# Kernel optimization log

Measured on AMD Instinct MI355X. Metric: run time of the kernel, lower is better.

## Reference

```python
import jax, jax.numpy as jnp
import numpy as np

B, D, N = 131072, 512, 101
BIG = 1e9
NORM_EPS = 0.1  # F.normalize eps


def setup_inputs() -> dict:
    key = jax.random.key(0)
    k1, k2, k3 = jax.random.split(key, 3)
    embeddings = jax.random.normal(k1, (B, D), dtype=jnp.float32)
    centers_weight = jax.random.normal(k2, (N, D), dtype=jnp.float32)
    labels = jax.random.randint(k3, (B,), 0, N, dtype=jnp.int64)
    return {"embeddings": embeddings, "centers_weight": centers_weight, "labels": labels}


def reference(embeddings, centers_weight, labels):
    # ---- center (MSE) term: per-sample squared distance to own center ----
    gathered = centers_weight[labels]                     # [B, D]
    center_loss = ((embeddings - gathered) ** 2).sum(axis=1)  # [B] (reduction=None)

    # ---- margin term (original operates on .data -> detached) ----
    W = jax.lax.stop_gradient(centers_weight)
    norms = jnp.sqrt((W * W).sum(axis=1, keepdims=True))
    C = W / jnp.maximum(norms, NORM_EPS)                  # F.normalize(p=2, eps=0.1)
    n = C.shape[0]
    dist = 1.0 - C @ C.T                                  # [N, N] cosine distance
    idx = jnp.arange(n)
    diff = jnp.abs(idx[:, None] - idx[None, :])
    dist = dist + BIG * (diff == 0)                       # mask diagonal (eye)

    # neighbor distances BEFORE they are masked out
    d_lower = jnp.diagonal(dist, offset=-1)               # Dist[i, i-1], i = 1..n-1
    d_upper = jnp.diagonal(dist, offset=1)                # Dist[i, i+1], i = 0..n-2

    dist_masked = dist + BIG * (diff == 1)                # mask adjacent centers
    min_dist = dist_masked.min(axis=1)                    # Dist[i, NegIdx]

    margin = (jax.nn.relu(2.0 * d_lower - min_dist[1:]).sum()
              + jax.nn.relu(2.0 * d_upper - min_dist[:-1]).sum()) / n

    return margin + center_loss.mean()
```

## Files before the change

kernel.cpp:

```cpp
#include <hip/hip_runtime.h>

#define BB 131072
#define DD 512
#define NN 101
#define D4 128
#define TOT (BB * D4)
#define GBLK 256
#define CBLK 2048
#define STR (CBLK * 256)
#define NPAIR (NN * NN)

typedef float f4 __attribute__((ext_vector_type(4)));

__global__ __launch_bounds__(256, 8) void fused_kernel(
    const f4* __restrict__ emb, const f4* __restrict__ ctr,
    const int* __restrict__ labels,
    float* __restrict__ partial,
    float* __restrict__ G)
{
    int lane = threadIdx.x & 63;
    int wid  = threadIdx.x >> 6;

    if (blockIdx.x < GBLK) {
        int w = blockIdx.x * 4 + wid;
        for (int p = w; p < NPAIR; p += GBLK * 4) {
            int i = p / NN;
            int j = p % NN;
            const f4* wi = ctr + i * D4;
            const f4* wj = ctr + j * D4;
            float dot = 0.f;
#pragma unroll
            for (int r = 0; r < 2; r++) {
                f4 a = wi[lane + r * 64];
                f4 c = wj[lane + r * 64];
                dot += a.x * c.x + a.y * c.y + a.z * c.z + a.w * c.w;
            }
            for (int off = 32; off > 0; off >>= 1)
                dot += __shfl_down(dot, off);
            if (lane == 0) G[p] = dot;
        }
        return;
    }

    int b   = blockIdx.x - GBLK;
    int tid = b * 256 + threadIdx.x;
    int d4  = tid & (D4 - 1);
    float local = 0.f;
#pragma unroll 1
    for (int kk = 0; kk < 8; kk++) {
        int i0 = tid + (kk * 4 + 0) * STR;
        int i1 = tid + (kk * 4 + 1) * STR;
        int i2 = tid + (kk * 4 + 2) * STR;
        int i3 = tid + (kk * 4 + 3) * STR;
        int l0 = labels[i0 >> 7];
        int l1 = labels[i1 >> 7];
        int l2 = labels[i2 >> 7];
        int l3 = labels[i3 >> 7];
        f4 e0 = emb[i0];
        f4 e1 = emb[i1];
        f4 e2 = emb[i2];
        f4 e3 = emb[i3];
        f4 c0 = ctr[l0 * D4 + d4];
        f4 c1 = ctr[l1 * D4 + d4];
        f4 c2 = ctr[l2 * D4 + d4];
        f4 c3 = ctr[l3 * D4 + d4];
        f4 t0 = e0 - c0;
        f4 t1 = e1 - c1;
        f4 t2 = e2 - c2;
        f4 t3 = e3 - c3;
        local += t0.x * t0.x + t0.y * t0.y + t0.z * t0.z + t0.w * t0.w;
        local += t1.x * t1.x + t1.y * t1.y + t1.z * t1.z + t1.w * t1.w;
        local += t2.x * t2.x + t2.y * t2.y + t2.z * t2.z + t2.w * t2.w;
        local += t3.x * t3.x + t3.y * t3.y + t3.z * t3.z + t3.w * t3.w;
    }
    for (int off = 32; off > 0; off >>= 1)
        local += __shfl_down(local, off);
    __shared__ float wsum[4];
    if (lane == 0) wsum[wid] = local;
    __syncthreads();
    if (threadIdx.x == 0)
        partial[b] = wsum[0] + wsum[1] + wsum[2] + wsum[3];
}

__global__ __launch_bounds__(256) void finalize_kernel(
    const float* __restrict__ G, const float* __restrict__ partial,
    float* __restrict__ out)
{
    int t = threadIdx.x;

    double dsum = 0.0;
    for (int i = t; i < CBLK; i += 256)
        dsum += (double)partial[i];
    for (int off = 32; off > 0; off >>= 1)
        dsum += __shfl_down(dsum, off);
    __shared__ double dacc[4];
    if ((t & 63) == 0) dacc[t >> 6] = dsum;

    __shared__ float denom[NN];
    __shared__ float mind[NN];
    if (t < NN)
        denom[t] = fmaxf(sqrtf(G[t * NN + t]), 0.1f);
    __syncthreads();
    if (t < NN) {
        float di = denom[t];
        float mn = 1e30f;
        for (int j = 0; j < NN; j++) {
            if (j >= t - 1 && j <= t + 1) continue;
            float d = 1.0f - G[t * NN + j] / (di * denom[j]);
            mn = fminf(mn, d);
        }
        mind[t] = mn;
    }
    __syncthreads();
    float contrib = 0.f;
    if (t >= 1 && t < NN) {
        float dl = 1.0f - G[t * NN + (t - 1)] / (denom[t] * denom[t - 1]);
        contrib += fmaxf(2.0f * dl - mind[t], 0.0f);
    }
    if (t < NN - 1) {
        float du = 1.0f - G[t * NN + (t + 1)] / (denom[t] * denom[t + 1]);
        contrib += fmaxf(2.0f * du - mind[t], 0.0f);
    }
    for (int off = 32; off > 0; off >>= 1)
        contrib += __shfl_down(contrib, off);
    __shared__ float wsum2[4];
    if ((t & 63) == 0) wsum2[t >> 6] = contrib;
    __syncthreads();
    if (t == 0) {
        float margin = (wsum2[0] + wsum2[1] + wsum2[2] + wsum2[3]) / (float)NN;
        double center = (dacc[0] + dacc[1] + dacc[2] + dacc[3]) / (double)BB;
        out[0] = margin + (float)center;
    }
}

extern "C" void kernel_launch(void* const* d_in, const int* in_sizes, int n_in,
                              void* d_out, int out_size, void* d_ws, size_t ws_size,
                              hipStream_t stream) {
    const float* emb    = (const float*)d_in[0];
    const float* ctr    = (const float*)d_in[1];
    const int*   labels = (const int*)d_in[2];
    float* out = (float*)d_out;

    float* partial = (float*)d_ws;
    float* G       = (float*)((char*)d_ws + CBLK * 4);

    fused_kernel<<<GBLK + CBLK, 256, 0, stream>>>(
        (const f4*)emb, (const f4*)ctr, labels, partial, G);
    finalize_kernel<<<1, 256, 0, stream>>>(G, partial, out);
}
```

Before: 76.70 us.

## Fold finalize into main kernel via last-block atomic gate and fixed-point accumulator

Removes the separate finalize kernel launch by having each block increment a global counter, with the last block computing the margin term and the final output. Per-block center sums are accumulated into a 64-bit fixed-point integer atomic instead of a partial array, and the margin min-reduction is parallelised over all pairs with ordered-uint atomicMin in shared memory. This adds a memset launch, a threadfence per block and atomics on a single address, and fixed-point scaling may lose precision or overflow.

```diff
diff --git a/kernel.cpp b/kernel.cpp
--- a/kernel.cpp
+++ b/kernel.cpp
@@ -7,16 +7,28 @@
 #define TOT (BB * D4)
 #define GBLK 256
 #define CBLK 2048
+#define TOTB (GBLK + CBLK)
 #define STR (CBLK * 256)
 #define NPAIR (NN * NN)
+#define SCALE 1048576.0
 
 typedef float f4 __attribute__((ext_vector_type(4)));
+
+__device__ __forceinline__ unsigned int fenc(float f) {
+    unsigned int u = __float_as_uint(f);
+    return ((int)u < 0) ? ~u : (u | 0x80000000u);
+}
+__device__ __forceinline__ float fdec(unsigned int k) {
+    return ((int)k < 0) ? __uint_as_float(k & 0x7FFFFFFFu) : __uint_as_float(~k);
+}
 
 __global__ __launch_bounds__(256, 8) void fused_kernel(
     const f4* __restrict__ emb, const f4* __restrict__ ctr,
     const int* __restrict__ labels,
-    float* __restrict__ partial,
-    float* __restrict__ G)
+    unsigned int* __restrict__ counter,
+    unsigned long long* __restrict__ acc,
+    float* __restrict__ G,
+    float* __restrict__ out)
 {
     int lane = threadIdx.x & 63;
     int wid  = threadIdx.x >> 6;
@@ -37,98 +49,100 @@
             }
             for (int off = 32; off > 0; off >>= 1)
                 dot += __shfl_down(dot, off);
-            if (lane == 0) G[p] = dot;
+            if (lane == 0) atomicExch(&G[p], dot);
         }
-        return;
+    } else {
+        int b   = blockIdx.x - GBLK;
+        int tid = b * 256 + threadIdx.x;
+        int d4  = tid & (D4 - 1);
+        float local = 0.f;
+#pragma unroll 1
+        for (int kk = 0; kk < 8; kk++) {
+            int i0 = tid + (kk * 4 + 0) * STR;
+            int i1 = tid + (kk * 4 + 1) * STR;
+            int i2 = tid + (kk * 4 + 2) * STR;
+            int i3 = tid + (kk * 4 + 3) * STR;
+            int l0 = labels[i0 >> 7];
+            int l1 = labels[i1 >> 7];
+            int l2 = labels[i2 >> 7];
+            int l3 = labels[i3 >> 7];
+            f4 e0 = emb[i0];
+            f4 e1 = emb[i1];
+            f4 e2 = emb[i2];
+            f4 e3 = emb[i3];
+            f4 c0 = ctr[l0 * D4 + d4];
+            f4 c1 = ctr[l1 * D4 + d4];
+            f4 c2 = ctr[l2 * D4 + d4];
+            f4 c3 = ctr[l3 * D4 + d4];
+            f4 t0 = e0 - c0;
+            f4 t1 = e1 - c1;
+            f4 t2 = e2 - c2;
+            f4 t3 = e3 - c3;
+            local += t0.x * t0.x + t0.y * t0.y + t0.z * t0.z + t0.w * t0.w;
+            local += t1.x * t1.x + t1.y * t1.y + t1.z * t1.z + t1.w * t1.w;
+            local += t2.x * t2.x + t2.y * t2.y + t2.z * t2.z + t2.w * t2.w;
+            local += t3.x * t3.x + t3.y * t3.y + t3.z * t3.z + t3.w * t3.w;
+        }
+        for (int off = 32; off > 0; off >>= 1)
+            local += __shfl_down(local, off);
+        __shared__ float wsum[4];
+        if (lane == 0) wsum[wid] = local;
+        __syncthreads();
+        if (threadIdx.x == 0) {
+            float s = wsum[0] + wsum[1] + wsum[2] + wsum[3];
+            atomicAdd(acc, (unsigned long long)(long long)((double)s * SCALE));
+        }
     }
 
-    int b   = blockIdx.x - GBLK;
-    int tid = b * 256 + threadIdx.x;
-    int d4  = tid & (D4 - 1);
-    float local = 0.f;
-#pragma unroll 1
-    for (int kk = 0; kk < 8; kk++) {
-        int i0 = tid + (kk * 4 + 0) * STR;
-        int i1 = tid + (kk * 4 + 1) * STR;
-        int i2 = tid + (kk * 4 + 2) * STR;
-        int i3 = tid + (kk * 4 + 3) * STR;
-        int l0 = labels[i0 >> 7];
-        int l1 = labels[i1 >> 7];
-        int l2 = labels[i2 >> 7];
-        int l3 = labels[i3 >> 7];
-        f4 e0 = emb[i0];
-        f4 e1 = emb[i1];
-        f4 e2 = emb[i2];
-        f4 e3 = emb[i3];
-        f4 c0 = ctr[l0 * D4 + d4];
-        f4 c1 = ctr[l1 * D4 + d4];
-        f4 c2 = ctr[l2 * D4 + d4];
-        f4 c3 = ctr[l3 * D4 + d4];
-        f4 t0 = e0 - c0;
-        f4 t1 = e1 - c1;
-        f4 t2 = e2 - c2;
-        f4 t3 = e3 - c3;
-        local += t0.x * t0.x + t0.y * t0.y + t0.z * t0.z + t0.w * t0.w;
-        local += t1.x * t1.x + t1.y * t1.y + t1.z * t1.z + t1.w * t1.w;
-        local += t2.x * t2.x + t2.y * t2.y + t2.z * t2.z + t2.w * t2.w;
-        local += t3.x * t3.x + t3.y * t3.y + t3.z * t3.z + t3.w * t3.w;
+    __syncthreads();
+    __shared__ unsigned int gate;
+    if (threadIdx.x == 0) {
+        __threadfence();
+        gate = atomicAdd(counter, 1u);
     }
-    for (int off = 32; off > 0; off >>= 1)
-        local += __shfl_down(local, off);
-    __shared__ float wsum[4];
-    if (lane == 0) wsum[wid] = local;
     __syncthreads();
-    if (threadIdx.x == 0)
-        partial[b] = wsum[0] + wsum[1] + wsum[2] + wsum[3];
-}
+    if (gate != TOTB - 1) return;
 
-__global__ __launch_bounds__(256) void finalize_kernel(
-    const float* __restrict__ G, const float* __restrict__ partial,
-    float* __restrict__ out)
-{
+    __shared__ float        denom[NN];
+    __shared__ unsigned int mbits[NN];
+    __shared__ float        dlow[NN];
+    __shared__ float        dupp[NN];
+    __shared__ float        fsum[4];
     int t = threadIdx.x;
 
-    double dsum = 0.0;
-    for (int i = t; i < CBLK; i += 256)
-        dsum += (double)partial[i];
-    for (int off = 32; off > 0; off >>= 1)
-        dsum += __shfl_down(dsum, off);
-    __shared__ double dacc[4];
-    if ((t & 63) == 0) dacc[t >> 6] = dsum;
-
-    __shared__ float denom[NN];
-    __shared__ float mind[NN];
-    if (t < NN)
-        denom[t] = fmaxf(sqrtf(G[t * NN + t]), 0.1f);
-    __syncthreads();
+    if (t < NN) mbits[t] = 0xFFFFFFFFu;
     if (t < NN) {
-        float di = denom[t];
-        float mn = 1e30f;
-        for (int j = 0; j < NN; j++) {
-            if (j >= t - 1 && j <= t + 1) continue;
-            float d = 1.0f - G[t * NN + j] / (di * denom[j]);
-            mn = fminf(mn, d);
-        }
-        mind[t] = mn;
+        float g = atomicAdd(&G[t * NN + t], 0.0f);
+        denom[t] = fmaxf(sqrtf(g), 0.1f);
     }
     __syncthreads();
+
+    for (int p = t; p < NPAIR; p += 256) {
+        int row = p / NN;
+        int col = p - row * NN;
+        float g = atomicAdd(&G[p], 0.0f);
+        float d = 1.0f - g / (denom[row] * denom[col]);
+        int diff = row - col;
+        if (diff > 1 || diff < -1)
+            atomicMin(&mbits[row], fenc(d));
+        else if (diff == 1)  dlow[row] = d;
+        else if (diff == -1) dupp[row] = d;
+    }
+    __syncthreads();
+
     float contrib = 0.f;
-    if (t >= 1 && t < NN) {
-        float dl = 1.0f - G[t * NN + (t - 1)] / (denom[t] * denom[t - 1]);
-        contrib += fmaxf(2.0f * dl - mind[t], 0.0f);
-    }
-    if (t < NN - 1) {
-        float du = 1.0f - G[t * NN + (t + 1)] / (denom[t] * denom[t + 1]);
-        contrib += fmaxf(2.0f * du - mind[t], 0.0f);
-    }
+    if (t >= 1 && t < NN)
+        contrib += fmaxf(2.0f * dlow[t] - fdec(mbits[t]), 0.0f);
+    if (t < NN - 1)
+        contrib += fmaxf(2.0f * dupp[t] - fdec(mbits[t]), 0.0f);
     for (int off = 32; off > 0; off >>= 1)
         contrib += __shfl_down(contrib, off);
-    __shared__ float wsum2[4];
-    if ((t & 63) == 0) wsum2[t >> 6] = contrib;
+    if ((t & 63) == 0) fsum[t >> 6] = contrib;
     __syncthreads();
     if (t == 0) {
-        float margin = (wsum2[0] + wsum2[1] + wsum2[2] + wsum2[3]) / (float)NN;
-        double center = (dacc[0] + dacc[1] + dacc[2] + dacc[3]) / (double)BB;
+        float margin = (fsum[0] + fsum[1] + fsum[2] + fsum[3]) / (float)NN;
+        unsigned long long a = atomicAdd(acc, 0ULL);
+        double center = (double)a / (SCALE * (double)BB);
         out[0] = margin + (float)center;
     }
 }
@@ -141,10 +155,11 @@
     const int*   labels = (const int*)d_in[2];
     float* out = (float*)d_out;
 
-    float* partial = (float*)d_ws;
-    float* G       = (float*)((char*)d_ws + CBLK * 4);
+    unsigned int*       counter = (unsigned int*)d_ws;
+    unsigned long long* acc     = (unsigned long long*)((char*)d_ws + 8);
+    float*              G       = (float*)((char*)d_ws + 64);
 
-    fused_kernel<<<GBLK + CBLK, 256, 0, stream>>>(
-        (const f4*)emb, (const f4*)ctr, labels, partial, G);
-    finalize_kernel<<<1, 256, 0, stream>>>(G, partial, out);
+    hipMemsetAsync(d_ws, 0, 16, stream);
+    fused_kernel<<<TOTB, 256, 0, stream>>>(
+        (const f4*)emb, (const f4*)ctr, labels, counter, acc, G, out);
 }
```

Measured after the change: 146.9 us. 91.5% more time.
